# Optimization experiments

Measured on AMD Instinct MI355X. Metric: run time of the kernel, lower is better.

The kernel has to match this reference:

```python
import jax, jax.numpy as jnp
import numpy as np

DIM = 4096
N_HEADS = 32
N_KV_HEADS = 8
HEAD_DIM = DIM // N_HEADS  # 128
SEQLEN = 2048
BATCH = 2
ROPE_THETA = 10000.0


def _precompute_freqs(seqlen, head_dim, theta):
    # matches torchtitan precompute_freqs_cis: freqs over even indices
    freqs = 1.0 / (theta ** (np.arange(0, head_dim, 2)[: head_dim // 2].astype(np.float32) / head_dim))
    t = np.arange(seqlen, dtype=np.float32)
    ang = np.outer(t, freqs)  # (S, head_dim//2)
    return jnp.asarray(np.cos(ang)), jnp.asarray(np.sin(ang))


def setup_inputs() -> dict:
    key = jax.random.key(0)
    kx, kq, kk, kv, ko = jax.random.split(key, 5)
    x = jax.random.normal(kx, (BATCH, SEQLEN, DIM), dtype=jnp.float32)
    wq = jax.random.normal(kq, (N_HEADS * HEAD_DIM, DIM), dtype=jnp.float32) * 0.02
    wk = jax.random.normal(kk, (N_KV_HEADS * HEAD_DIM, DIM), dtype=jnp.float32) * 0.02
    wv = jax.random.normal(kv, (N_KV_HEADS * HEAD_DIM, DIM), dtype=jnp.float32) * 0.02
    wo = jax.random.normal(ko, (DIM, N_HEADS * HEAD_DIM), dtype=jnp.float32) * 0.02
    cos, sin = _precompute_freqs(SEQLEN, HEAD_DIM, ROPE_THETA)
    return {"x": x, "cos": cos, "sin": sin, "wq": wq, "wk": wk, "wv": wv, "wo": wo}


def _apply_rope(t, cos, sin):
    # t: (B, S, H, hd); pairs (t[...,2i], t[...,2i+1]) rotated by angle
    tr = t.reshape(*t.shape[:-1], -1, 2)
    a, b = tr[..., 0], tr[..., 1]
    c = cos[None, :, None, :]  # (1, S, 1, hd//2)
    s = sin[None, :, None, :]
    out = jnp.stack([a * c - b * s, a * s + b * c], axis=-1)
    return out.reshape(t.shape)


def reference(x, cos, sin, wq, wk, wv, wo):
    B, S, D = x.shape
    hd = 2 * cos.shape[-1]
    H = wq.shape[0] // hd
    KVH = wk.shape[0] // hd
    n_rep = H // KVH

    q = (x @ wq.T).reshape(B, S, H, hd)
    k = (x @ wk.T).reshape(B, S, KVH, hd)
    v = (x @ wv.T).reshape(B, S, KVH, hd)

    q = _apply_rope(q, cos, sin)
    k = _apply_rope(k, cos, sin)

    # GQA: repeat_interleave kv heads (kept implicit via reshape of q into groups)
    qg = q.reshape(B, S, KVH, n_rep, hd)
    scale = 1.0 / jnp.sqrt(jnp.asarray(hd, dtype=x.dtype))
    # scores: (B, KVH, n_rep, S_q, S_k)
    scores = jnp.einsum("bsgrd,btgd->bgrst", qg, k) * scale
    causal = jnp.tril(jnp.ones((S, S), dtype=bool))
    scores = jnp.where(causal[None, None, None], scores, jnp.asarray(-1e30, dtype=scores.dtype))
    probs = jax.nn.softmax(scores, axis=-1)
    out = jnp.einsum("bgrst,btgd->bsgrd", probs, v).reshape(B, S, H * hd)
    return out @ wo.T
```

## Files before the change

### kernel.cpp

```cpp
#include <hip/hip_runtime.h>
#include <hip/hip_bf16.h>
#include <stdint.h>

#define DIM    4096
#define NH     32
#define NKVH   8
#define HD     128
#define SEQ    2048
#define BATCH  2
#define MTOT   (BATCH*SEQ)
#define SCALE  0.08838834764831845f

typedef __bf16 bf16_t;
typedef __bf16 bf16x8 __attribute__((ext_vector_type(8)));
typedef float  f32x4  __attribute__((ext_vector_type(4)));

#define AS1 __attribute__((address_space(1)))
#define AS3 __attribute__((address_space(3)))

__device__ __forceinline__ void gload_lds16(const void* g, void* l) {
    __builtin_amdgcn_global_load_lds((const AS1 void*)g, (AS3 void*)l, 16, 0, 0);
}

__device__ __forceinline__ void fence_barrier() {
    asm volatile("" ::: "memory");
    __builtin_amdgcn_s_barrier();
    asm volatile("" ::: "memory");
}

__global__ __launch_bounds__(256)
void cvt_f32_bf16(const float* __restrict__ in, bf16_t* __restrict__ out, int n4) {
    for (int i = blockIdx.x * blockDim.x + threadIdx.x; i < n4;
         i += gridDim.x * blockDim.x) {
        float4 v = reinterpret_cast<const float4*>(in)[i];
        union { bf16_t b[4]; uint2 u; } t;
        t.b[0] = (bf16_t)v.x; t.b[1] = (bf16_t)v.y;
        t.b[2] = (bf16_t)v.z; t.b[3] = (bf16_t)v.w;
        reinterpret_cast<uint2*>(out)[i] = t.u;
    }
}

__global__ __launch_bounds__(256)
void cvt_weights(const float* __restrict__ wq, const float* __restrict__ wk,
                 const float* __restrict__ wv, const float* __restrict__ wo,
                 bf16_t* __restrict__ out) {
    const int n0 = DIM * DIM / 4;
    const int n1 = NKVH * HD * DIM / 4;
    const int n2 = NKVH * HD * DIM / 4;
    const int n3 = DIM * DIM / 4;
    const int ntot = n0 + n1 + n2 + n3;
    for (int i = blockIdx.x * blockDim.x + threadIdx.x; i < ntot;
         i += gridDim.x * blockDim.x) {
        const float* src;
        int k = i;
        if (k < n0) src = wq;
        else if ((k -= n0) < n1) src = wk;
        else if ((k -= n1) < n2) src = wv;
        else { k -= n2; src = wo; }
        float4 v = reinterpret_cast<const float4*>(src)[k];
        union { bf16_t b[4]; uint2 u; } t;
        t.b[0] = (bf16_t)v.x; t.b[1] = (bf16_t)v.y;
        t.b[2] = (bf16_t)v.z; t.b[3] = (bf16_t)v.w;
        reinterpret_cast<uint2*>(out)[i] = t.u;
    }
}


__device__ __forceinline__ void stage_half(const bf16_t* gbase, int kt, int h,
                                           bf16_t* ldsdst, int tid, int w) {
#pragma unroll
    for (int t2 = 0; t2 < 2; ++t2) {
        int s = t2 * 512 + tid;
        int r = s >> 3, c = s & 7;
        gload_lds16(gbase + (size_t)(h * 128 + r) * DIM + kt + ((c ^ (r & 7)) * 8),
                    ldsdst + (size_t)(t2 * 512 + w * 64) * 8);
    }
}

__device__ __forceinline__ void read_a4(bf16x8 a[4][2], const bf16_t* Ahalf,
                                        int mh, int lr, int lg) {
#pragma unroll
    for (int mi = 0; mi < 4; ++mi) {
        int r = mh * 64 + mi * 16 + lr;
#pragma unroll
        for (int kk = 0; kk < 2; ++kk)
            a[mi][kk] = *(const bf16x8*)(Ahalf + r * 64 + ((kk * 4 + lg) ^ (r & 7)) * 8);
    }
}

__device__ __forceinline__ void read_b2(bf16x8 b[2][2], const bf16_t* Bhalf,
                                        int np, int rb, int lg) {
#pragma unroll
    for (int ni = 0; ni < 2; ++ni) {
        int r = rb + (np * 2 + ni) * 16;
#pragma unroll
        for (int kk = 0; kk < 2; ++kk)
            b[ni][kk] = *(const bf16x8*)(Bhalf + r * 64 + ((kk * 4 + lg) ^ (r & 7)) * 8);
    }
}

template<int MODE>
__global__ __launch_bounds__(512, 2)
void gemm8(const bf16_t* __restrict__ A,
           const bf16_t* __restrict__ B0,
           float* __restrict__ outF,
           bf16_t* __restrict__ outQ,
           bf16_t* __restrict__ outK,
           bf16_t* __restrict__ outV,
           const float* __restrict__ cosT,
           const float* __restrict__ sinT) {
    __shared__ __align__(16) bf16_t As[2][2][128 * 64];
    __shared__ __align__(16) bf16_t Bs[2][2][128 * 64];

    const int tid = threadIdx.x;
    const int l = tid & 63;
    const int w = tid >> 6;
    const int wm = w >> 2, wn = w & 3;
    const int lr = l & 15, lg = l >> 4;
    const int rb = (wn & 1) * 64 + lr;

    constexpr int NY = (MODE == 3) ? 24 : 16;
    const int nwg = 16 * NY;
    const int bid = blockIdx.y * gridDim.x + blockIdx.x;
    const int swz = (bid & 7) * (nwg >> 3) + (bid >> 3);
    const int bx = swz / NY;
    const int ct = swz - bx * NY;
    const int rowBase = bx * 256;

    const bf16_t* Ap = A + (size_t)rowBase * DIM;
    const bf16_t* Bp = B0 + (size_t)ct * 256 * DIM;

    f32x4 acc[8][4] = {};
    bf16x8 aq[4][2];
    bf16x8 bA[2][2];
    bf16x8 bB[2][2];

    const int NT = DIM / 64;

    stage_half(Bp, 0,  0, &Bs[0][0][0], tid, w);
    stage_half(Bp, 0,  1, &Bs[0][1][0], tid, w);
    stage_half(Ap, 0,  0, &As[0][0][0], tid, w);
    stage_half(Ap, 0,  1, &As[0][1][0], tid, w);
    stage_half(Bp, 64, 0, &Bs[1][0][0], tid, w);
    stage_half(Bp, 64, 1, &Bs[1][1][0], tid, w);
    asm volatile("s_waitcnt vmcnt(4)" ::: "memory");
    fence_barrier();

    for (int j = 0; j < NT; ++j) {
        const int s = j & 1;
        const bf16_t* Ah = &As[s][wm][0];
        const bf16_t* Bh = &Bs[s][wn >> 1][0];
        const int ktA = ((j + 1 < NT) ? j + 1 : NT - 1) * 64;
        const int ktB = ((j + 2 < NT) ? j + 2 : NT - 1) * 64;

        read_a4(aq, Ah, 0, lr, lg);
        read_b2(bA, Bh, 0, rb, lg);
        stage_half(Ap, ktA, 0, &As[s ^ 1][0][0], tid, w);
        asm volatile("s_waitcnt lgkmcnt(8)" ::: "memory");
        fence_barrier();
        asm volatile("s_waitcnt lgkmcnt(0)" ::: "memory");
        __builtin_amdgcn_s_setprio(1);
#pragma unroll
        for (int kk = 0; kk < 2; ++kk)
#pragma unroll
            for (int mi = 0; mi < 4; ++mi) {
                acc[mi][0] = __builtin_amdgcn_mfma_f32_16x16x32_bf16(aq[mi][kk], bA[0][kk], acc[mi][0], 0, 0, 0);
                acc[mi][1] = __builtin_amdgcn_mfma_f32_16x16x32_bf16(aq[mi][kk], bA[1][kk], acc[mi][1], 0, 0, 0);
            }
        __builtin_amdgcn_s_setprio(0);
        fence_barrier();

        read_b2(bB, Bh, 1, rb, lg);
        stage_half(Ap, ktA, 1, &As[s ^ 1][1][0], tid, w);
        fence_barrier();
        asm volatile("s_waitcnt lgkmcnt(0)" ::: "memory");
        __builtin_amdgcn_s_setprio(1);
#pragma unroll
        for (int kk = 0; kk < 2; ++kk)
#pragma unroll
            for (int mi = 0; mi < 4; ++mi) {
                acc[mi][2] = __builtin_amdgcn_mfma_f32_16x16x32_bf16(aq[mi][kk], bB[0][kk], acc[mi][2], 0, 0, 0);
                acc[mi][3] = __builtin_amdgcn_mfma_f32_16x16x32_bf16(aq[mi][kk], bB[1][kk], acc[mi][3], 0, 0, 0);
            }
        __builtin_amdgcn_s_setprio(0);
        fence_barrier();

        read_a4(aq, Ah, 1, lr, lg);
        stage_half(Bp, ktB, 0, &Bs[s][0][0], tid, w);
        fence_barrier();
        asm volatile("s_waitcnt lgkmcnt(0)" ::: "memory");
        __builtin_amdgcn_s_setprio(1);
#pragma unroll
        for (int kk = 0; kk < 2; ++kk)
#pragma unroll
            for (int mi = 0; mi < 4; ++mi) {
                acc[mi + 4][0] = __builtin_amdgcn_mfma_f32_16x16x32_bf16(aq[mi][kk], bA[0][kk], acc[mi + 4][0], 0, 0, 0);
                acc[mi + 4][1] = __builtin_amdgcn_mfma_f32_16x16x32_bf16(aq[mi][kk], bA[1][kk], acc[mi + 4][1], 0, 0, 0);
            }
        __builtin_amdgcn_s_setprio(0);
        fence_barrier();

        stage_half(Bp, ktB, 1, &Bs[s][1][0], tid, w);
        fence_barrier();
        __builtin_amdgcn_s_setprio(1);
#pragma unroll
        for (int kk = 0; kk < 2; ++kk)
#pragma unroll
            for (int mi = 0; mi < 4; ++mi) {
                acc[mi + 4][2] = __builtin_amdgcn_mfma_f32_16x16x32_bf16(aq[mi][kk], bB[0][kk], acc[mi + 4][2], 0, 0, 0);
                acc[mi + 4][3] = __builtin_amdgcn_mfma_f32_16x16x32_bf16(aq[mi][kk], bB[1][kk], acc[mi + 4][3], 0, 0, 0);
            }
        __builtin_amdgcn_s_setprio(0);
        asm volatile("s_waitcnt vmcnt(4)" ::: "memory");
        fence_barrier();
    }

#pragma unroll
    for (int mi = 0; mi < 8; ++mi) {
        int gmBase = rowBase + wm * 128 + mi * 16 + lg * 4;
#pragma unroll
        for (int ni = 0; ni < 4; ++ni) {
            f32x4 v4 = acc[mi][ni];
            int gn = ct * 256 + wn * 64 + ni * 16 + lr;
            if (MODE == 0) {
#pragma unroll
                for (int i = 0; i < 4; ++i)
                    outF[(size_t)(gmBase + i) * DIM + gn] = v4[i];
            } else {
                if (ct < 16) {
                    int h = gn >> 7, d = gn & 127, pi2 = d >> 1;
#pragma unroll
                    for (int i = 0; i < 4; ++i) {
                        float v = v4[i];
                        float pvv = __shfl_xor(v, 1);
                        int gm = gmBase + i;
                        int bb = gm >> 11, sidx = gm & (SEQ - 1);
                        float c = cosT[sidx * 64 + pi2], sn = sinT[sidx * 64 + pi2];
                        float o = (d & 1) ? (pvv * sn + v * c) : (v * c - pvv * sn);
                        outQ[((size_t)(bb * NH + h) * SEQ + sidx) * HD + d] = (bf16_t)o;
                    }
                } else if (ct < 20) {
                    int kn = gn - 4096;
                    int h = kn >> 7, d = kn & 127, pi2 = d >> 1;
#pragma unroll
                    for (int i = 0; i < 4; ++i) {
                        float v = v4[i];
                        float pvv = __shfl_xor(v, 1);
                        int gm = gmBase + i;
                        int bb = gm >> 11, sidx = gm & (SEQ - 1);
                        float c = cosT[sidx * 64 + pi2], sn = sinT[sidx * 64 + pi2];
                        float o = (d & 1) ? (pvv * sn + v * c) : (v * c - pvv * sn);
                        outK[((size_t)(bb * NKVH + h) * SEQ + sidx) * HD + d] = (bf16_t)o;
                    }
                } else {
                    int vn = gn - 5120;
                    int kvh = vn >> 7, d = vn & 127;
#pragma unroll
                    for (int i = 0; i < 4; ++i) {
                        float dummy = __shfl_xor(v4[i], 1); (void)dummy;
                        int gm = gmBase + i;
                        int bb = gm >> 11, sidx = gm & (SEQ - 1);
                        outV[((size_t)(bb * NKVH + kvh) * HD + d) * SEQ + sidx] = (bf16_t)v4[i];
                    }
                }
            }
        }
    }
}

__global__ __launch_bounds__(256, 2)
void attn_fwd(const bf16_t* __restrict__ Qr,
              const bf16_t* __restrict__ Kr,
              const bf16_t* __restrict__ Vt,
              bf16_t* __restrict__ Ob) {
    __shared__ __align__(16) bf16_t Ks[2][64 * 128];
    __shared__ __align__(16) bf16_t Vs[2][128 * 64];
    __shared__ __align__(16) bf16_t Ps[4][32 * 64];

    const int tid = threadIdx.x;
    const int l  = tid & 63;
    const int w  = tid >> 6;
    const int lr = l & 15, lg = l >> 4;
    const int e  = lr & 7;

    const int qt  = 15 - (blockIdx.x >> 6);
    const int bh  = blockIdx.x & 63;
    const int b   = bh >> 5;
    const int h   = bh & 31;
    const int kvh = h >> 2;
    const int q0  = qt * 128;
    const int nt  = 2 * qt + 2;
    const int qmin = q0 + w * 32;

    const bf16_t* kbase = Kr + (size_t)(b * NKVH + kvh) * SEQ * HD;
    const bf16_t* vbase = Vt + (size_t)(b * NKVH + kvh) * HD * SEQ;

    bf16x8 qf[2][4];
    const bf16_t* qp = Qr + ((size_t)(b * NH + h) * SEQ + qmin + lr) * HD;
#pragma unroll
    for (int mi = 0; mi < 2; ++mi)
#pragma unroll
        for (int kk = 0; kk < 4; ++kk)
            qf[mi][kk] = *(const bf16x8*)(qp + (size_t)mi * 16 * HD + kk * 32 + lg * 8);

    f32x4 oacc[2][8] = {};
    float mrow[2] = {-1e30f, -1e30f};
    float lsum[2] = {0.f, 0.f};

#pragma unroll
    for (int t2 = 0; t2 < 4; ++t2) {
        int s = t2 * 256 + tid;
        { int r = s >> 4, g = (s & 15) ^ (r & 7);
          gload_lds16(kbase + (size_t)r * HD + g * 8,
                      &Ks[0][(size_t)(t2 * 256 + w * 64) * 8]); }
        { int r = s >> 3, g = (s & 7) ^ (r & 7);
          gload_lds16(vbase + (size_t)r * SEQ + g * 8,
                      &Vs[0][(size_t)(t2 * 256 + w * 64) * 8]); }
    }
    __syncthreads();

    int cur = 0;
    for (int t = 0; t < nt; ++t) {
        if (t + 1 < nt) {
            const int kv1 = (t + 1) * 64;
#pragma unroll
            for (int t2 = 0; t2 < 4; ++t2) {
                int s = t2 * 256 + tid;
                { int r = s >> 4, g = (s & 15) ^ (r & 7);
                  gload_lds16(kbase + (size_t)(kv1 + r) * HD + g * 8,
                              &Ks[cur ^ 1][(size_t)(t2 * 256 + w * 64) * 8]); }
                { int r = s >> 3, g = (s & 7) ^ (r & 7);
                  gload_lds16(vbase + (size_t)r * SEQ + kv1 + g * 8,
                              &Vs[cur ^ 1][(size_t)(t2 * 256 + w * 64) * 8]); }
            }
        }

        const bool active = (t * 64) <= (qmin + 31);
        if (active) {
            const bool needMask = (t * 64 + 63) > qmin;

            f32x4 sf[2][4] = {};
#pragma unroll
            for (int kk = 0; kk < 4; ++kk)
#pragma unroll
                for (int nf = 0; nf < 4; ++nf) {
                    bf16x8 kf = *(const bf16x8*)(
                        &Ks[cur][(nf * 16 + lr) * 128 + ((kk * 4 + lg) ^ e) * 8]);
#pragma unroll
                    for (int mi = 0; mi < 2; ++mi)
                        sf[mi][nf] = __builtin_amdgcn_mfma_f32_16x16x32_bf16(
                            kf, qf[mi][kk], sf[mi][nf], 0, 0, 0);
                }

            float aO[2][4];
#pragma unroll
            for (int mi = 0; mi < 2; ++mi) {
                const int qrow = qmin + mi * 16 + lr;
                float mt = -1e30f;
#pragma unroll
                for (int nf = 0; nf < 4; ++nf)
#pragma unroll
                    for (int i = 0; i < 4; ++i) {
                        float sc = sf[mi][nf][i] * SCALE;
                        if (needMask && (t * 64 + nf * 16 + lg * 4 + i) > qrow)
                            sc = -1e30f;
                        sf[mi][nf][i] = sc;
                        mt = fmaxf(mt, sc);
                    }
                mt = fmaxf(mt, __shfl_xor(mt, 16));
                mt = fmaxf(mt, __shfl_xor(mt, 32));
                float mnew = fmaxf(mrow[mi], mt);
                float alpha = __expf(mrow[mi] - mnew);
                mrow[mi] = mnew;
                float rs = 0.f;
#pragma unroll
                for (int nf = 0; nf < 4; ++nf)
#pragma unroll
                    for (int i = 0; i < 4; ++i) {
                        float p = __expf(sf[mi][nf][i] - mnew);
                        sf[mi][nf][i] = p;
                        rs += p;
                    }
                rs += __shfl_xor(rs, 16);
                rs += __shfl_xor(rs, 32);
                lsum[mi] = lsum[mi] * alpha + rs;
#pragma unroll
                for (int i = 0; i < 4; ++i)
                    aO[mi][i] = __shfl(alpha, lg * 4 + i);
            }

#pragma unroll
            for (int mi = 0; mi < 2; ++mi)
#pragma unroll
                for (int df = 0; df < 8; ++df)
#pragma unroll
                    for (int i = 0; i < 4; ++i)
                        oacc[mi][df][i] *= aO[mi][i];

#pragma unroll
            for (int mi = 0; mi < 2; ++mi)
#pragma unroll
                for (int nf = 0; nf < 4; ++nf) {
                    union { bf16_t bb[4]; uint2 u; } pk;
#pragma unroll
                    for (int i = 0; i < 4; ++i) pk.bb[i] = (bf16_t)sf[mi][nf][i];
                    int addr = (mi * 16 + lr) * 64 +
                               (((nf * 2 + (lg >> 1)) ^ e) << 3) + (lg & 1) * 4;
                    *(uint2*)(&Ps[w][addr]) = pk.u;
                }
            asm volatile("s_waitcnt lgkmcnt(0)" ::: "memory");
            __builtin_amdgcn_sched_barrier(0);

            bf16x8 pf[2][2];
#pragma unroll
            for (int mi = 0; mi < 2; ++mi)
#pragma unroll
                for (int k2 = 0; k2 < 2; ++k2)
                    pf[mi][k2] = *(const bf16x8*)(
                        &Ps[w][(mi * 16 + lr) * 64 + ((k2 * 4 + lg) ^ e) * 8]);
#pragma unroll
            for (int df = 0; df < 8; ++df)
#pragma unroll
                for (int k2 = 0; k2 < 2; ++k2) {
                    bf16x8 vf = *(const bf16x8*)(
                        &Vs[cur][(df * 16 + lr) * 64 + ((k2 * 4 + lg) ^ e) * 8]);
#pragma unroll
                    for (int mi = 0; mi < 2; ++mi)
                        oacc[mi][df] = __builtin_amdgcn_mfma_f32_16x16x32_bf16(
                            pf[mi][k2], vf, oacc[mi][df], 0, 0, 0);
                }
        }
        __syncthreads();
        cur ^= 1;
    }

#pragma unroll
    for (int mi = 0; mi < 2; ++mi) {
        float ls[4];
#pragma unroll
        for (int i = 0; i < 4; ++i)
            ls[i] = 1.f / __shfl(lsum[mi], lg * 4 + i);
#pragma unroll
        for (int df = 0; df < 8; ++df)
#pragma unroll
            for (int i = 0; i < 4; ++i) {
                float o = oacc[mi][df][i] * ls[i];
                int gm = b * SEQ + qmin + mi * 16 + lg * 4 + i;
                int gn = h * HD + df * 16 + lr;
                Ob[(size_t)gm * DIM + gn] = (bf16_t)o;
            }
    }
}

extern "C" void kernel_launch(void* const* d_in, const int* in_sizes, int n_in,
                              void* d_out, int out_size, void* d_ws, size_t ws_size,
                              hipStream_t stream) {
    const float* x    = (const float*)d_in[0];
    const float* cosT = (const float*)d_in[1];
    const float* sinT = (const float*)d_in[2];
    const float* wq   = (const float*)d_in[3];
    const float* wk   = (const float*)d_in[4];
    const float* wv   = (const float*)d_in[5];
    const float* wo   = (const float*)d_in[6];

    bf16_t* p = (bf16_t*)d_ws;
    bf16_t* xb  = p; p += (size_t)MTOT * DIM;
    bf16_t* wb  = p; p += (size_t)(DIM + 2 * NKVH * HD + DIM) * DIM;
    bf16_t* Qr  = p; p += (size_t)MTOT * DIM;
    bf16_t* Kr  = p; p += (size_t)BATCH * NKVH * SEQ * HD;
    bf16_t* Vt  = p; p += (size_t)BATCH * NKVH * HD * SEQ;
    bf16_t* Ob  = p; p += (size_t)MTOT * DIM;

    bf16_t* wob = wb + (size_t)(DIM + 2 * NKVH * HD) * DIM;

    cvt_f32_bf16<<<2048, 256, 0, stream>>>(x, xb, MTOT * DIM / 4);
    cvt_weights<<<2048, 256, 0, stream>>>(wq, wk, wv, wo, wb);

    gemm8<3><<<dim3(16, 24), 512, 0, stream>>>(
        xb, wb, nullptr, Qr, Kr, Vt, cosT, sinT);

    attn_fwd<<<1024, 256, 0, stream>>>(Qr, Kr, Vt, Ob);

    gemm8<0><<<dim3(16, 16), 512, 0, stream>>>(
        Ob, wob, (float*)d_out, nullptr, nullptr, nullptr, nullptr, nullptr);
}
```

Before: 576.1 us.

## Software-pipeline LDS fragment reads across GEMM phases and drop block swizzle

Restructures the GEMM main loop so each LDS fragment read is issued one phase ahead of its MFMA consumer. Double-buffered A registers (a0/a1) and a prefetch of the next tile's first fragments at the end of each iteration let the LDS reads overlap with matrix math, and several barriers are removed. The change also drops the XCD/L2 block-index swizzle in favour of direct blockIdx mapping, which may hurt L2 locality. It raises register pressure and makes the barrier/waitcnt ordering more delicate.

```diff
diff --git a/kernel.cpp b/kernel.cpp
--- a/kernel.cpp
+++ b/kernel.cpp
@@ -118,22 +118,17 @@
     const int wm = w >> 2, wn = w & 3;
     const int lr = l & 15, lg = l >> 4;
     const int rb = (wn & 1) * 64 + lr;
-
-    constexpr int NY = (MODE == 3) ? 24 : 16;
-    const int nwg = 16 * NY;
-    const int bid = blockIdx.y * gridDim.x + blockIdx.x;
-    const int swz = (bid & 7) * (nwg >> 3) + (bid >> 3);
-    const int bx = swz / NY;
-    const int ct = swz - bx * NY;
-    const int rowBase = bx * 256;
+    const int bh2 = wn >> 1;
+
+    const int rowBase = blockIdx.x * 256;
+    const int ct = blockIdx.y;
 
     const bf16_t* Ap = A + (size_t)rowBase * DIM;
     const bf16_t* Bp = B0 + (size_t)ct * 256 * DIM;
 
     f32x4 acc[8][4] = {};
-    bf16x8 aq[4][2];
-    bf16x8 bA[2][2];
-    bf16x8 bB[2][2];
+    bf16x8 a0[4][2], a1[4][2];
+    bf16x8 bA[2][2], bB[2][2];
 
     const int NT = DIM / 64;
 
@@ -145,74 +140,73 @@
     stage_half(Bp, 64, 1, &Bs[1][1][0], tid, w);
     asm volatile("s_waitcnt vmcnt(4)" ::: "memory");
     fence_barrier();
+    read_a4(a0, &As[0][wm][0], 0, lr, lg);
+    read_b2(bA, &Bs[0][bh2][0], 0, rb, lg);
 
     for (int j = 0; j < NT; ++j) {
         const int s = j & 1;
         const bf16_t* Ah = &As[s][wm][0];
-        const bf16_t* Bh = &Bs[s][wn >> 1][0];
+        const bf16_t* Bh = &Bs[s][bh2][0];
         const int ktA = ((j + 1 < NT) ? j + 1 : NT - 1) * 64;
         const int ktB = ((j + 2 < NT) ? j + 2 : NT - 1) * 64;
 
-        read_a4(aq, Ah, 0, lr, lg);
-        read_b2(bA, Bh, 0, rb, lg);
+        read_b2(bB, Bh, 1, rb, lg);
         stage_half(Ap, ktA, 0, &As[s ^ 1][0][0], tid, w);
+        asm volatile("s_waitcnt lgkmcnt(4)" ::: "memory");
+        __builtin_amdgcn_s_setprio(1);
+#pragma unroll
+        for (int kk = 0; kk < 2; ++kk)
+#pragma unroll
+            for (int mi = 0; mi < 4; ++mi) {
+                acc[mi][0] = __builtin_amdgcn_mfma_f32_16x16x32_bf16(a0[mi][kk], bA[0][kk], acc[mi][0], 0, 0, 0);
+                acc[mi][1] = __builtin_amdgcn_mfma_f32_16x16x32_bf16(a0[mi][kk], bA[1][kk], acc[mi][1], 0, 0, 0);
+            }
+        __builtin_amdgcn_s_setprio(0);
+        fence_barrier();
+
+        read_a4(a1, Ah, 1, lr, lg);
+        stage_half(Ap, ktA, 1, &As[s ^ 1][1][0], tid, w);
         asm volatile("s_waitcnt lgkmcnt(8)" ::: "memory");
+        __builtin_amdgcn_s_setprio(1);
+#pragma unroll
+        for (int kk = 0; kk < 2; ++kk)
+#pragma unroll
+            for (int mi = 0; mi < 4; ++mi) {
+                acc[mi][2] = __builtin_amdgcn_mfma_f32_16x16x32_bf16(a0[mi][kk], bB[0][kk], acc[mi][2], 0, 0, 0);
+                acc[mi][3] = __builtin_amdgcn_mfma_f32_16x16x32_bf16(a0[mi][kk], bB[1][kk], acc[mi][3], 0, 0, 0);
+            }
+        __builtin_amdgcn_s_setprio(0);
         fence_barrier();
+
+        stage_half(Bp, ktB, 0, &Bs[s][0][0], tid, w);
         asm volatile("s_waitcnt lgkmcnt(0)" ::: "memory");
         __builtin_amdgcn_s_setprio(1);
 #pragma unroll
         for (int kk = 0; kk < 2; ++kk)
 #pragma unroll
             for (int mi = 0; mi < 4; ++mi) {
-                acc[mi][0] = __builtin_amdgcn_mfma_f32_16x16x32_bf16(aq[mi][kk], bA[0][kk], acc[mi][0], 0, 0, 0);
-                acc[mi][1] = __builtin_amdgcn_mfma_f32_16x16x32_bf16(aq[mi][kk], bA[1][kk], acc[mi][1], 0, 0, 0);
+                acc[mi + 4][0] = __builtin_amdgcn_mfma_f32_16x16x32_bf16(a1[mi][kk], bA[0][kk], acc[mi + 4][0], 0, 0, 0);
+                acc[mi + 4][1] = __builtin_amdgcn_mfma_f32_16x16x32_bf16(a1[mi][kk], bA[1][kk], acc[mi + 4][1], 0, 0, 0);
             }
         __builtin_amdgcn_s_setprio(0);
         fence_barrier();
 
-        read_b2(bB, Bh, 1, rb, lg);
-        stage_half(Ap, ktA, 1, &As[s ^ 1][1][0], tid, w);
-        fence_barrier();
-        asm volatile("s_waitcnt lgkmcnt(0)" ::: "memory");
+        stage_half(Bp, ktB, 1, &Bs[s][1][0], tid, w);
         __builtin_amdgcn_s_setprio(1);
 #pragma unroll
         for (int kk = 0; kk < 2; ++kk)
 #pragma unroll
             for (int mi = 0; mi < 4; ++mi) {
-                acc[mi][2] = __builtin_amdgcn_mfma_f32_16x16x32_bf16(aq[mi][kk], bB[0][kk], acc[mi][2], 0, 0, 0);
-                acc[mi][3] = __builtin_amdgcn_mfma_f32_16x16x32_bf16(aq[mi][kk], bB[1][kk], acc[mi][3], 0, 0, 0);
-            }
-        __builtin_amdgcn_s_setprio(0);
-        fence_barrier();
-
-        read_a4(aq, Ah, 1, lr, lg);
-        stage_half(Bp, ktB, 0, &Bs[s][0][0], tid, w);
-        fence_barrier();
-        asm volatile("s_waitcnt lgkmcnt(0)" ::: "memory");
-        __builtin_amdgcn_s_setprio(1);
-#pragma unroll
-        for (int kk = 0; kk < 2; ++kk)
-#pragma unroll
-            for (int mi = 0; mi < 4; ++mi) {
-                acc[mi + 4][0] = __builtin_amdgcn_mfma_f32_16x16x32_bf16(aq[mi][kk], bA[0][kk], acc[mi + 4][0], 0, 0, 0);
-                acc[mi + 4][1] = __builtin_amdgcn_mfma_f32_16x16x32_bf16(aq[mi][kk], bA[1][kk], acc[mi + 4][1], 0, 0, 0);
-            }
-        __builtin_amdgcn_s_setprio(0);
-        fence_barrier();
-
-        stage_half(Bp, ktB, 1, &Bs[s][1][0], tid, w);
-        fence_barrier();
-        __builtin_amdgcn_s_setprio(1);
-#pragma unroll
-        for (int kk = 0; kk < 2; ++kk)
-#pragma unroll
-            for (int mi = 0; mi < 4; ++mi) {
-                acc[mi + 4][2] = __builtin_amdgcn_mfma_f32_16x16x32_bf16(aq[mi][kk], bB[0][kk], acc[mi + 4][2], 0, 0, 0);
-                acc[mi + 4][3] = __builtin_amdgcn_mfma_f32_16x16x32_bf16(aq[mi][kk], bB[1][kk], acc[mi + 4][3], 0, 0, 0);
+                acc[mi + 4][2] = __builtin_amdgcn_mfma_f32_16x16x32_bf16(a1[mi][kk], bB[0][kk], acc[mi + 4][2], 0, 0, 0);
+                acc[mi + 4][3] = __builtin_amdgcn_mfma_f32_16x16x32_bf16(a1[mi][kk], bB[1][kk], acc[mi + 4][3], 0, 0, 0);
             }
         __builtin_amdgcn_s_setprio(0);
         asm volatile("s_waitcnt vmcnt(4)" ::: "memory");
         fence_barrier();
+        if (j + 1 < NT) {
+            read_a4(a0, &As[s ^ 1][wm][0], 0, lr, lg);
+            read_b2(bA, &Bs[s ^ 1][bh2][0], 0, rb, lg);
+        }
     }
 
 #pragma unroll
```

Measured after the change: 517.0 us. 10.3% less time.
